# Kernel tuning notes

Hardware: AMD Instinct MI355X
Metric: run time of the kernel (lower is better)

## Reference

```python
import jax, jax.numpy as jnp
import numpy as np

# ---- problem constants (from init_kwargs) ----
R = 64
NX = 16384
NV = 2048
LX = 2.0
LV = 16.0
DX = LX / NX
DV = LV / NV
VS = (jnp.arange(NV, dtype=jnp.float32) + 0.5) * DV - LV / 2.0  # cell-centered v grid
AE, AI = 1.0, 100.0
ZE, ZI = -1.0, 1.0
OMEGA_C_TAU = 1.0
DT = 1e-3
SPECIES = ('electron', 'ion')
ZS = {'electron': ZE, 'ion': ZI}
AS = {'electron': AE, 'ion': AI}


def _minmod(a, b):
    return jnp.where(a * b > 0, jnp.where(jnp.abs(a) < jnp.abs(b), a, b), 0.0)


def slope_limited_flux_divergence(u, flux_func, dh):
    """u: (r, N+4) with 2 ghost cells each side; returns (r, N) flux divergence."""
    du = jnp.diff(u, axis=1)                    # (r, N+3)
    sigma = _minmod(du[:, :-1], du[:, 1:])      # slopes for cells 1..N+2, (r, N+2)
    uc = u[:, 1:-1]                             # cells 1..N+2
    left = uc[:, :-1] + 0.5 * sigma[:, :-1]     # interface states (r, N+1)
    right = uc[:, 1:] - 0.5 * sigma[:, 1:]
    F = flux_func(left, right)                  # (r, N+1)
    return (F[:, 1:] - F[:, :-1]) / dh


def apply_absorbing_wall_bcs(K, V, n_ghost):
    # V @ diag(indicator) @ V.T expressed as column-scaled GEMM
    Vm = (V * jnp.where(VS < 0, 1.0, 0.0)[None, :]) @ V.T * DV  # (r,r)
    Vp = (V * jnp.where(VS > 0, 1.0, 0.0)[None, :]) @ V.T * DV
    if n_ghost == 1:
        return jnp.concatenate([Vm @ K[:, :1], K, Vp @ K[:, -1:]], axis=1)
    return jnp.concatenate([Vm @ K[:, [1, 0]], K, Vp @ K[:, [-1, -2]]], axis=1)


def rho_c_species(X, S, V, Z):
    mass = V @ jnp.ones(NV, dtype=V.dtype) * DV   # (r,)
    return Z * (X.T @ (S @ mass))                  # (Nx,)


def poisson_solve(rho):
    # Periodic spectral Poisson: dE/dx = rho  ->  E_hat = rho_hat / (i k)
    k = 2.0 * jnp.pi * jnp.fft.fftfreq(NX, d=DX)
    rh = jnp.fft.fft(rho)
    Eh = jnp.where(k != 0, rh / (1j * k), 0.0)
    return jnp.real(jnp.fft.ifft(Eh)).astype(rho.dtype)


def solve_poisson(ys):
    rho = (rho_c_species(*ys['electron'], ZE) + rho_c_species(*ys['ion'], ZI))
    return poisson_solve(rho)


def ssprk2(y, f, dt):
    f0 = f(y)
    y1 = jax.tree.map(lambda a, b: a + dt * b, y, f0)
    f1 = f(y1)
    return jax.tree.map(lambda a, b, c: 0.5 * (a + b + dt * c), y, y1, f1)


def _vpm_matrices(V):
    vp = jnp.where(VS > 0, VS, 0.0)
    vm = jnp.where(VS < 0, VS, 0.0)
    v_plus = (V * vp[None, :]) @ V.T * DV
    v_minus = (V * vm[None, :]) @ V.T * DV
    return v_plus, v_minus


def _V_lr_matrices(V):
    dV = jnp.diff(V, axis=1) / DV
    zc = jnp.zeros((R, 1), dtype=V.dtype)
    V_left = V @ jnp.concatenate([zc, dV], axis=1).T * DV
    V_right = V @ jnp.concatenate([dV, zc], axis=1).T * DV
    return V_left, V_right


def K_rhs(K, V, E, Z, A):
    v_plus, v_minus = _vpm_matrices(V)
    V_left, V_right = _V_lr_matrices(V)
    Ep = jnp.where(E > 0, E, 0.0)[None, :]
    Em = jnp.where(E < 0, E, 0.0)[None, :]
    Kb = apply_absorbing_wall_bcs(K, V, 2)
    v_flux = slope_limited_flux_divergence(
        Kb, lambda l, r: v_plus @ l + v_minus @ r, DX)
    fac = OMEGA_C_TAU * Z / A
    E_flux = fac * (V_left @ (K * Ep) + V_right @ (K * Em))
    return -v_flux - E_flux


def _K_lr_matrices(X, S, V):
    K = apply_absorbing_wall_bcs((X.T @ S).T, V, 1)   # (r, Nx+2)
    Kdl = jnp.diff(K[:, :-1], axis=1) / DX            # (r, Nx)
    Kdr = jnp.diff(K[:, 1:], axis=1) / DX
    K_left = X @ Kdl.T * DX                           # (r, r)
    K_right = X @ Kdr.T * DX
    return K_left, K_right


def S_rhs(S, X, V, E, Z, A):
    v_plus, v_minus = _vpm_matrices(V)
    K_left, K_right = _K_lr_matrices(X, S, V)
    v_term = K_left @ v_plus.T + K_right @ v_minus.T
    V_left, V_right = _V_lr_matrices(V)
    Ep_mat = (X * jnp.where(E > 0, E, 0.0)[None, :]) @ X.T * DX
    Em_mat = (X * jnp.where(E < 0, E, 0.0)[None, :]) @ X.T * DX
    fac = OMEGA_C_TAU * Z / A
    E_term = fac * (Ep_mat @ S @ V_left.T + Em_mat @ S @ V_right.T)
    return v_term + E_term


def L_rhs(L, X, E, Z, A):
    Vt, S = jnp.linalg.qr(L.T)          # L.T: (Nv, r)
    S = S * DV ** 0.5
    V = Vt.T / DV ** 0.5
    K_left, K_right = _K_lr_matrices(X, S, V)
    vp = jnp.where(VS > 0, VS, 0.0)[None, :]
    vm = jnp.where(VS < 0, VS, 0.0)[None, :]
    v_flux = vp * (K_left @ V) + vm * (K_right @ V)
    fac = OMEGA_C_TAU * Z / A
    Ef = fac * E
    Ep_mat = (X * jnp.where(Ef > 0, Ef, 0.0)[None, :]) @ X.T * DX
    Em_mat = (X * jnp.where(Ef < 0, Ef, 0.0)[None, :]) @ X.T * DX
    Lb = jnp.pad(L, [(0, 0), (2, 2)])   # ghost cells (zeros in lieu of mode='empty')
    E_flux = slope_limited_flux_divergence(
        Lb, lambda l, r: Ep_mat @ l + Em_mat @ r, DV)
    return -v_flux - E_flux


def step(ys):
    # --- K step ---
    E = solve_poisson(ys)
    Ks = {sp: (ys[sp][0].T @ ys[sp][1]).T for sp in SPECIES}
    Ks = ssprk2(Ks, lambda Ks: {sp: K_rhs(Ks[sp], ys[sp][2], E, ZS[sp], AS[sp])
                                for sp in SPECIES}, DT)
    new = {}
    for sp in SPECIES:
        Xt, S = jnp.linalg.qr(Ks[sp].T)
        new[sp] = (Xt.T / DX ** 0.5, S * DX ** 0.5, ys[sp][2])
    ys = new
    # --- S step ---
    E = solve_poisson(ys)
    Ss = {sp: ys[sp][1] for sp in SPECIES}
    Ss = ssprk2(Ss, lambda Ss: {sp: S_rhs(Ss[sp], ys[sp][0], ys[sp][2], E, ZS[sp], AS[sp])
                                for sp in SPECIES}, DT)
    ys = {sp: (ys[sp][0], Ss[sp], ys[sp][2]) for sp in SPECIES}
    # --- L step ---
    E = solve_poisson(ys)
    Ls = {sp: ys[sp][1] @ ys[sp][2] for sp in SPECIES}
    Ls = ssprk2(Ls, lambda Ls: {sp: L_rhs(Ls[sp], ys[sp][0], E, ZS[sp], AS[sp])
                                for sp in SPECIES}, DT)
    new = {}
    for sp in SPECIES:
        Vt, S = jnp.linalg.qr(Ls[sp].T)
        new[sp] = (ys[sp][0], S * DV ** 0.5, Vt.T / DV ** 0.5)
    return new


def _ortho_rows(key, r, n, dh):
    A = jax.random.normal(key, (n, r), dtype=jnp.float32)
    Q, _ = jnp.linalg.qr(A)
    return Q.T / jnp.sqrt(dh)   # rows orthonormal w.r.t. trapezoid weight dh


def setup_inputs() -> dict:
    key = jax.random.key(0)
    ks = jax.random.split(key, 6)
    Xe = _ortho_rows(ks[0], R, NX, DX)
    Ve = _ortho_rows(ks[1], R, NV, DV)
    Xi = _ortho_rows(ks[2], R, NX, DX)
    Vi = _ortho_rows(ks[3], R, NV, DV)
    Se = 0.1 * jnp.eye(R, dtype=jnp.float32) + 0.01 * jax.random.normal(ks[4], (R, R), dtype=jnp.float32)
    Si = 0.1 * jnp.eye(R, dtype=jnp.float32) + 0.01 * jax.random.normal(ks[5], (R, R), dtype=jnp.float32)
    return {'Xe': Xe, 'Se': Se, 'Ve': Ve, 'Xi': Xi, 'Si': Si, 'Vi': Vi}


def reference(Xe, Se, Ve, Xi, Si, Vi):
    ys = {'electron': (Xe, Se, Ve), 'ion': (Xi, Si, Vi)}
    ys = step(ys)
    return (ys['electron'][0], ys['electron'][1], ys['electron'][2],
            ys['ion'][0], ys['ion'][1], ys['ion'][2])
```

## Files before the change

### kernel.cpp

```cpp
#include <hip/hip_runtime.h>

#define R 64
#define NX 16384
#define NV 2048
#define NXP (NX+8)
#define NVP (NV+8)
#define TW 64
#define SPLIT_VM 8
#define SPLIT_X 64
#define SPLIT_QRX 128
#define SPLIT_QRV 32

#define DXf 1.220703125e-4f
#define DVf 0.0078125f
#define DTf 0.001f
#define PI_F 3.14159265358979323846f
#define FAC_E (-1.0f)
#define FAC_I (0.01f)
#define ZE_F (-1.0f)
#define ZI_F (1.0f)
#define SQRT_DXf 0.011048543456039806f
#define SQRT_DVf 0.08838834764831845f
#define ISQRT_DXf 90.50966799187808f
#define ISQRT_DVf 11.313708498984761f

#define X_OFF 0
#define V_OFF 1048576
#define S_OFF 1179648
#define S1_OFF 1183744
#define SQ_OFF 1187840
#define D_OFF 1191936
#define MATS_OFF 1196032
#define SM_OFF 1228800
#define GLR_OFF 1245184
#define R1IF_OFF 1269760
#define KA_OFF 1277952
#define KB_OFF 2327040
#define LA_OFF KB_OFF
#define LB_OFF (KB_OFF+131584)
#define VQ_OFF (KB_OFF+394240)
#define PART_OFF 3376128
#define PARTQR_OFF PART_OFF
#define GD_OFF 4686848
#define SPS 4695040
#define RHO_OFF 9390080
#define E_OFF 9406464
#define C_OFF 9422848
#define FFT1_OFF 9426944
#define FFT2_OFF 9459712
#define DOUT_SPS 1183744
#define DOUT_X 0
#define DOUT_S 1048576
#define DOUT_V 1052672

__device__ __forceinline__ float mm2(float a, float b) {
    return (a*b > 0.0f) ? ((fabsf(a) < fabsf(b)) ? a : b) : 0.0f;
}

__global__ __launch_bounds__(256) void k_gram(float* W, int mode, int a_off, int lda,
    int e_abs, float fac0, float fac1, int out_off, int N, int nsplit)
{
  int sp = blockIdx.z, mat = blockIdx.y, split = blockIdx.x;
  float* base = W + (size_t)sp*SPS;
  const float* A = base + a_off;
  float fac = sp ? fac1 : fac0;
  float* outp = base + out_off + (size_t)(mat*nsplit + split)*4096;
  int chunk = N / nsplit;
  int xb0 = split * chunk;
  __shared__ float tA[TW][R+1], tB[TW][R+1];
  float acc[4][4] = {};
  int tid = threadIdx.x, ty = tid >> 4, tx = tid & 15;
  for (int xt = 0; xt < chunk; xt += TW) {
    for (int idx = tid; idx < TW*R; idx += 256) {
      int xi = idx & 63, r = idx >> 6;
      int x = xb0 + xt + xi;
      float av, bv;
      if (mode == 0) {
        float vv = A[(size_t)r*lda + x];
        float vs = ((float)x + 0.5f)*DVf - 8.0f;
        if (mat == 0)      { av = vv * (fmaxf(vs,0.f)*DVf); bv = vv; }
        else if (mat == 1) { av = vv * (fminf(vs,0.f)*DVf); bv = vv; }
        else if (mat == 2) { av = vv * ((vs<0.f)?DVf:0.f); bv = vv; }
        else if (mat == 3) { av = vv * ((vs>0.f)?DVf:0.f); bv = vv; }
        else if (mat == 4) { av = vv; bv = (x>=1)   ? (vv - A[(size_t)r*lda + x-1]) : 0.f; }
        else               { av = vv; bv = (x<NV-1) ? (A[(size_t)r*lda + x+1] - vv) : 0.f; }
      } else if (mode == 1) {
        float vv = A[(size_t)r*lda + x];
        float vs = ((float)x + 0.5f)*DVf - 8.0f;
        float w = (mat==0) ? ((vs<0.f)?DVf:0.f) : ((vs>0.f)?DVf:0.f);
        av = vv*w; bv = vv;
      } else if (mode == 3) {
        float e = W[e_abs + x] * fac;
        float vv = A[(size_t)r*lda + x];
        av = vv * (((mat==0) ? fmaxf(e,0.f) : fminf(e,0.f)) * DXf);
        bv = vv;
      } else {
        float vv = A[(size_t)r*lda + x];
        av = vv;
        if (mat == 0) bv = (x>=1)  ? (vv - A[(size_t)r*lda + x-1]) : vv;
        else          bv = (x<N-1) ? (A[(size_t)r*lda + x+1] - vv) : -vv;
      }
      tA[xi][r] = av; tB[xi][r] = bv;
    }
    __syncthreads();
    for (int xi = 0; xi < TW; ++xi) {
      float a0 = tA[xi][ty*4+0], a1 = tA[xi][ty*4+1], a2 = tA[xi][ty*4+2], a3 = tA[xi][ty*4+3];
      float b0 = tB[xi][tx*4+0], b1 = tB[xi][tx*4+1], b2 = tB[xi][tx*4+2], b3 = tB[xi][tx*4+3];
      acc[0][0]+=a0*b0; acc[0][1]+=a0*b1; acc[0][2]+=a0*b2; acc[0][3]+=a0*b3;
      acc[1][0]+=a1*b0; acc[1][1]+=a1*b1; acc[1][2]+=a1*b2; acc[1][3]+=a1*b3;
      acc[2][0]+=a2*b0; acc[2][1]+=a2*b1; acc[2][2]+=a2*b2; acc[2][3]+=a2*b3;
      acc[3][0]+=a3*b0; acc[3][1]+=a3*b1; acc[3][2]+=a3*b2; acc[3][3]+=a3*b3;
    }
    __syncthreads();
  }
  #pragma unroll
  for (int i = 0; i < 4; ++i)
    #pragma unroll
    for (int j = 0; j < 4; ++j)
      outp[(ty*4+i)*64 + tx*4 + j] = acc[i][j];
}

__global__ __launch_bounds__(256) void k_gram_qr(float* W, int a_off, int lda, int aoff,
    int N, int nsplit, int outd_off)
{
  int sp = blockIdx.z, split = blockIdx.x;
  float* base = W + (size_t)sp*SPS;
  const float* A = base + a_off + aoff;
  double* outp = (double*)(base + outd_off) + (size_t)split*4096;
  int chunk = N / nsplit, x0 = split*chunk;
  __shared__ float tA[TW][R+1];
  double acc[4][4] = {};
  int tid = threadIdx.x, ty = tid >> 4, tx = tid & 15;
  for (int xt = 0; xt < chunk; xt += TW) {
    for (int idx = tid; idx < TW*R; idx += 256) {
      int xi = idx & 63, r = idx >> 6;
      tA[xi][r] = A[(size_t)r*lda + x0 + xt + xi];
    }
    __syncthreads();
    for (int xi = 0; xi < TW; ++xi) {
      double a0 = tA[xi][ty*4+0], a1 = tA[xi][ty*4+1], a2 = tA[xi][ty*4+2], a3 = tA[xi][ty*4+3];
      double b0 = tA[xi][tx*4+0], b1 = tA[xi][tx*4+1], b2 = tA[xi][tx*4+2], b3 = tA[xi][tx*4+3];
      acc[0][0]+=a0*b0; acc[0][1]+=a0*b1; acc[0][2]+=a0*b2; acc[0][3]+=a0*b3;
      acc[1][0]+=a1*b0; acc[1][1]+=a1*b1; acc[1][2]+=a1*b2; acc[1][3]+=a1*b3;
      acc[2][0]+=a2*b0; acc[2][1]+=a2*b1; acc[2][2]+=a2*b2; acc[2][3]+=a2*b3;
      acc[3][0]+=a3*b0; acc[3][1]+=a3*b1; acc[3][2]+=a3*b2; acc[3][3]+=a3*b3;
    }
    __syncthreads();
  }
  #pragma unroll
  for (int i = 0; i < 4; ++i)
    #pragma unroll
    for (int j = 0; j < 4; ++j)
      outp[(ty*4+i)*64 + tx*4 + j] = acc[i][j];
}

__global__ __launch_bounds__(256) void k_reduce2(float* W, int src_off, int dst_off, int nsplit)
{
  int sp = blockIdx.z, mat = blockIdx.x;
  int e = blockIdx.y*256 + threadIdx.x;
  float* base = W + (size_t)sp*SPS;
  const float* src = base + src_off + (size_t)mat*nsplit*4096 + e;
  float s = 0;
  for (int k = 0; k < nsplit; ++k) s += src[(size_t)k*4096];
  base[dst_off + (size_t)mat*4096 + e] = s;
}

__global__ __launch_bounds__(256) void k_reduced(float* W, int src_off, int dst_off, int nsplit)
{
  int sp = blockIdx.z;
  int e = blockIdx.x*256 + threadIdx.x;
  float* base = W + (size_t)sp*SPS;
  const double* src = (const double*)(base + src_off) + e;
  double s = 0;
  for (int k = 0; k < nsplit; ++k) s += src[(size_t)k*4096];
  ((double*)(base + dst_off))[e] = s;
}

__global__ __launch_bounds__(256) void k_rr(float* W, int a_off, int transA, int b_off,
    int ldb, int boff, int c_off, int ldc, int coff, int d_off, float alpha,
    float* dout, int dmir_off)
{
  int sp = blockIdx.z;
  float* base = W + (size_t)sp*SPS;
  const float* A = base + a_off;
  const float* B = base + b_off + boff;
  float* C = base + c_off + coff;
  float* M = (dmir_off >= 0) ? (dout + (size_t)sp*DOUT_SPS + dmir_off) : nullptr;
  __shared__ float tA[R][R+1];
  __shared__ float dsc[R];
  int tid = threadIdx.x;
  for (int idx = tid; idx < R*R; idx += 256) {
    int r = idx >> 6, j = idx & 63;
    tA[r][j] = transA ? A[j*R + r] : A[idx];
  }
  if (tid < R) dsc[tid] = (d_off >= 0) ? base[d_off + tid] : 1.0f;
  __syncthreads();
  int ty = tid >> 4, tx = tid & 15;
  int x0 = blockIdx.x*64 + tx*4;
  float acc[4][4] = {};
  for (int r = 0; r < R; ++r) {
    float4 bv = *(const float4*)(B + (size_t)r*ldb + x0);
    float a0 = tA[r][ty*4+0], a1 = tA[r][ty*4+1], a2 = tA[r][ty*4+2], a3 = tA[r][ty*4+3];
    acc[0][0]+=a0*bv.x; acc[0][1]+=a0*bv.y; acc[0][2]+=a0*bv.z; acc[0][3]+=a0*bv.w;
    acc[1][0]+=a1*bv.x; acc[1][1]+=a1*bv.y; acc[1][2]+=a1*bv.z; acc[1][3]+=a1*bv.w;
    acc[2][0]+=a2*bv.x; acc[2][1]+=a2*bv.y; acc[2][2]+=a2*bv.z; acc[2][3]+=a2*bv.w;
    acc[3][0]+=a3*bv.x; acc[3][1]+=a3*bv.y; acc[3][2]+=a3*bv.z; acc[3][3]+=a3*bv.w;
  }
  #pragma unroll
  for (int i = 0; i < 4; ++i) {
    int j = ty*4 + i;
    float s = alpha * dsc[j];
    float4 o = make_float4(acc[i][0]*s, acc[i][1]*s, acc[i][2]*s, acc[i][3]*s);
    *(float4*)(C + (size_t)j*ldc + x0) = o;
    if (M) *(float4*)(M + (size_t)j*ldc + x0) = o;
  }
}

__global__ __launch_bounds__(256) void k_ghost2(float* W, int k_off)
{
  int sp = blockIdx.z;
  float* base = W + (size_t)sp*SPS;
  float* K = base + k_off;
  int tid = threadIdx.x;
  int j = tid & 63, c = tid >> 6;
  const float* M = base + MATS_OFF + ((c < 2) ? 2 : 3)*4096;
  int dst = (c==0)?2 : (c==1)?3 : (c==2)?(NX+4):(NX+5);
  int src = (c==0)?5 : (c==1)?4 : (c==2)?(NX+3):(NX+2);
  float s = 0;
  for (int m = 0; m < R; ++m) s += M[j*R + m] * K[(size_t)m*NXP + src];
  K[(size_t)j*NXP + dst] = s;
}

__global__ __launch_bounds__(256) void k_ghostL(float* W)
{
  int sp = blockIdx.z;
  float* base = W + (size_t)sp*SPS;
  for (int idx = threadIdx.x; idx < 512; idx += 256) {
    int which = idx >> 8; int r = (idx >> 2) & 63; int c = idx & 3;
    int col = (c < 2) ? (2 + c) : (NV + 4 + (c - 2));
    (base + (which ? LB_OFF : LA_OFF))[(size_t)r*NVP + col] = 0.f;
  }
}

__global__ __launch_bounds__(256) void k_flux(float* W, int U_off, int Kx_off, int ldkx,
    int kxoff, int useWin, int P_off, int Mi_off, int A2_off, int B2_off,
    int e_abs, float fac0, float fac1, float dh_inv, int N, int ldp,
    int stage, int orig_off, int out_off)
{
  int sp = blockIdx.z;
  float* base = W + (size_t)sp*SPS;
  const float* U  = base + U_off;
  const float* Kx = base + Kx_off;
  const float* Pm = base + P_off;
  const float* Mm = base + Mi_off;
  const float* Am = base + A2_off;
  const float* Bm = base + B2_off;
  float fac = sp ? fac1 : fac0;
  int x0 = blockIdx.x * 32;
  __shared__ float win[R][37];
  __shared__ float dLt[32][R+1];
  __shared__ float dRt[32][R+1];
  __shared__ float KTt[32][R+1];
  int tid = threadIdx.x;
  for (int idx = tid; idx < R*36; idx += 256) {
    int c = idx % 36, m = idx / 36;
    win[m][c] = U[(size_t)m*ldp + x0 + 2 + c];
  }
  __syncthreads();
  for (int idx = tid; idx < R*32; idx += 256) {
    int xi = idx & 31, m = idx >> 5;
    float u0 = win[m][xi], u1 = win[m][xi+1], u2 = win[m][xi+2], u3 = win[m][xi+3], u4 = win[m][xi+4];
    float d01 = u1-u0, d12 = u2-u1, d23 = u3-u2, d34 = u4-u3;
    float s1 = mm2(d01,d12), s2 = mm2(d12,d23), s3 = mm2(d23,d34);
    dLt[xi][m] = ((u2 + 0.5f*s2) - (u1 + 0.5f*s1)) * dh_inv;
    dRt[xi][m] = ((u3 - 0.5f*s3) - (u2 - 0.5f*s2)) * dh_inv;
    KTt[xi][m] = useWin ? u2 : Kx[(size_t)m*ldkx + kxoff + x0 + xi];
  }
  __syncthreads();
  int ty = tid >> 4, tx = tid & 15;
  int j0 = ty*4;
  float aP[4][2] = {}, aM[4][2] = {}, aA[4][2] = {}, aB[4][2] = {};
  for (int m = 0; m < R; ++m) {
    float dl0 = dLt[tx*2][m],   dl1 = dLt[tx*2+1][m];
    float dr0 = dRt[tx*2][m],   dr1 = dRt[tx*2+1][m];
    float kt0 = KTt[tx*2][m],   kt1 = KTt[tx*2+1][m];
    #pragma unroll
    for (int i = 0; i < 4; ++i) {
      float p = Pm[(j0+i)*R + m], q = Mm[(j0+i)*R + m];
      float a = Am[(j0+i)*R + m], b = Bm[(j0+i)*R + m];
      aP[i][0] += p*dl0; aP[i][1] += p*dl1;
      aM[i][0] += q*dr0; aM[i][1] += q*dr1;
      aA[i][0] += a*kt0; aA[i][1] += a*kt1;
      aB[i][0] += b*kt0; aB[i][1] += b*kt1;
    }
  }
  const float* orig = base + orig_off;
  float* out = base + out_off;
  for (int xx = 0; xx < 2; ++xx) {
    int x = x0 + tx*2 + xx;
    float w1, w2;
    if (e_abs >= 0) { float e = W[e_abs + x]; w1 = fac*fmaxf(e,0.f); w2 = fac*fminf(e,0.f); }
    else { float vs = ((float)x + 0.5f)*DVf - 8.0f; w1 = fmaxf(vs,0.f); w2 = fminf(vs,0.f); }
    #pragma unroll
    for (int i = 0; i < 4; ++i) {
      int j = j0 + i;
      float rhs = -(aP[i][xx] + aM[i][xx] + w1*aA[i][xx] + w2*aB[i][xx]);
      float uval = win[j][tx*2 + xx + 2];
      float res;
      if (stage == 1) res = uval + DTf*rhs;
      else res = 0.5f*(orig[(size_t)j*ldp + 4 + x] + uval + DTf*rhs);
      out[(size_t)j*ldp + 4 + x] = res;
    }
  }
}

__global__ __launch_bounds__(512) void k_cholA(float* W, int gd_off,
    int a_off, int lda, int aoff, int sout_off, float sscale,
    float* dout, int dmir_off)
{
  int sp = blockIdx.z;
  float* base = W + (size_t)sp*SPS;
  const double* GD = (const double*)(base + gd_off);
  const float* A = base + a_off + aoff;
  float* Rinv = base + R1IF_OFF;
  __shared__ double G[R][R+1];
  __shared__ double Wi[R][R+1];
  __shared__ double T[R][R+1];
  __shared__ float  As[R][R+1];
  __shared__ double Pb[32][33];
  __shared__ double red[8][R];
  __shared__ double dinv[R];
  __shared__ double dsh[R];
  int tid = threadIdx.x;
  int j = tid & 63, q = tid >> 6;
  for (int e = tid; e < 4096; e += 512) {
    G[e>>6][e&63] = GD[e];
    As[e>>6][e&63] = A[(size_t)(e>>6)*lda + (e&63)];
  }
  __syncthreads();
  for (int k = 0; k < R; ++k) {
    if (j > k) {
      double gkj = G[k][j] / G[k][k];
      for (int i = k+1+q; i <= j; i += 8) G[i][j] -= G[k][i]*gkj;
    }
    __syncthreads();
  }
  if (tid < R) dinv[tid] = 1.0 / sqrt(G[tid][tid]);
  __syncthreads();
  for (int i = q; i <= j; i += 8) G[i][j] *= dinv[i];
  __syncthreads();
  if (q == 0) Wi[j][j] = dinv[j];
  __syncthreads();
  int blo = j & 32;
  for (int t = 1; t < 32; ++t) {
    int i = j - t;
    double s = 0;
    if (i >= blo) {
      for (int m = i+1+q; m <= j; m += 8) s += G[i][m]*Wi[m][j];
    }
    red[q][j] = s;
    __syncthreads();
    if (q == 0 && i >= blo)
      Wi[i][j] = -(red[0][j]+red[1][j]+red[2][j]+red[3][j]
                  +red[4][j]+red[5][j]+red[6][j]+red[7][j]) * dinv[i];
    __syncthreads();
  }
  for (int u = 0; u < 2; ++u) {
    int e = tid + 512*u;
    int m = e >> 5, jj = 32 + (e & 31);
    double s = 0;
    for (int k2 = 32; k2 <= jj; ++k2) s += G[m][k2]*Wi[k2][jj];
    Pb[m][jj-32] = s;
  }
  __syncthreads();
  for (int u = 0; u < 2; ++u) {
    int e = tid + 512*u;
    int i = e >> 5, jj = 32 + (e & 31);
    double s = 0;
    for (int m = i; m < 32; ++m) s += Wi[i][m]*Pb[m][jj-32];
    Wi[i][jj] = -s;
  }
  __syncthreads();
  for (int e = tid; e < 4096; e += 512) {
    int i = e>>6, jj = e&63;
    Rinv[e] = (i<=jj) ? (float)Wi[i][jj] : 0.0f;
  }
  for (int x = q; x < R; x += 8) {
    double s = 0;
    for (int m = 0; m <= j; ++m) s += Wi[m][j]*(double)As[m][x];
    T[x][j] = s;
  }
  __syncthreads();
  for (int k = 0; k < R; ++k) {
    double tkk = T[k][k];
    double d = (tkk >= 0.0) ? -1.0 : 1.0;
    if (tid == k) dsh[k] = d;
    if (j > k) {
      double c = d * T[k][j] / (1.0 + fabs(tkk));
      for (int m = k+1+q; m < R; m += 8) T[m][j] += c * T[m][k];
    }
    __syncthreads();
  }
  if (tid < 64) base[D_OFF + tid] = (float)dsh[tid];
  float* mir = (dmir_off >= 0) ? (dout + (size_t)sp*DOUT_SPS + dmir_off) : nullptr;
  for (int e = tid; e < 4096; e += 512) {
    int i = e >> 6, jj = e & 63;
    float v = (i <= jj) ? (float)(dsh[i] * G[i][jj] * (double)sscale) : 0.0f;
    base[sout_off + e] = v;
    if (mir) mir[e] = v;
  }
}

__global__ __launch_bounds__(256) void k_klr(float* W, int s_off, int vm_idx, int vp_idx)
{
  int sp = blockIdx.x;
  float* base = W + (size_t)sp*SPS;
  __shared__ float Cb[4096];
  __shared__ float x0s[R], x1s[R], u0[R], u1[R], g0[R], g1[R];
  int tid = threadIdx.x, ty = tid>>4, tx = tid&15;
  const float* Sin = base + s_off;
  for (int e = tid; e < 4096; e += 256) Cb[e] = Sin[e];
  if (tid < R) { x0s[tid] = base[X_OFF + (size_t)tid*NX]; x1s[tid] = base[X_OFF + (size_t)tid*NX + NX-1]; }
  __syncthreads();
  if (tid < R) {
    float s0=0,s1=0;
    for (int m=0;m<R;++m){ float c=Cb[m*64+tid]; s0+=c*x0s[m]; s1+=c*x1s[m]; }
    u0[tid]=s0; u1[tid]=s1;
  }
  __syncthreads();
  if (tid < R) {
    const float* Vm = base + MATS_OFF + vm_idx*4096;
    const float* Vp = base + MATS_OFF + vp_idx*4096;
    float s0=0,s1=0;
    for (int c=0;c<R;++c){ s0+=Vm[tid*64+c]*u0[c]; s1+=Vp[tid*64+c]*u1[c]; }
    g0[tid]=s0; g1[tid]=s1;
  }
  __syncthreads();
  const float* GLg = base + GLR_OFF;
  const float* GRg = base + GLR_OFF + 4096;
  float aKL[4][4]={}, aKR[4][4]={};
  for (int m=0;m<R;++m) {
    float gl[4], gr[4], cj[4];
    #pragma unroll
    for (int i=0;i<4;++i){ gl[i]=GLg[(ty*4+i)*64+m]; gr[i]=GRg[(ty*4+i)*64+m]; }
    #pragma unroll
    for (int j=0;j<4;++j) cj[j]=Cb[m*64+tx*4+j];
    #pragma unroll
    for (int i=0;i<4;++i)
      #pragma unroll
      for (int j=0;j<4;++j){ aKL[i][j]+=gl[i]*cj[j]; aKR[i][j]+=gr[i]*cj[j]; }
  }
  #pragma unroll
  for (int i=0;i<4;++i)
    #pragma unroll
    for (int j=0;j<4;++j){
      int e=(ty*4+i)*64+tx*4+j;
      base[SM_OFF+e]      = aKL[i][j] - x0s[ty*4+i]*g0[tx*4+j];
      base[SM_OFF+4096+e] = aKR[i][j] + x1s[ty*4+i]*g1[tx*4+j];
    }
}

__global__ __launch_bounds__(256) void k_sstep(float* W, int stage)
{
  int sp = blockIdx.x;
  float* base = W + (size_t)sp*SPS;
  float fac = sp ? FAC_I : FAC_E;
  __shared__ float Ab[4096], Bb[4096], Cb[4096];
  __shared__ float x0s[R], x1s[R], u0[R], u1[R], g0[R], g1[R];
  int tid = threadIdx.x, ty = tid >> 4, tx = tid & 15;
  const float* Sin = base + ((stage==1)? S_OFF : S1_OFF);
  for (int e = tid; e < 4096; e += 256) Cb[e] = Sin[e];
  if (tid < R) { x0s[tid] = base[X_OFF + (size_t)tid*NX]; x1s[tid] = base[X_OFF + (size_t)tid*NX + NX-1]; }
  __syncthreads();
  if (tid < R) {
    float s0=0,s1=0;
    for (int m=0;m<R;++m){ float c=Cb[m*64+tid]; s0+=c*x0s[m]; s1+=c*x1s[m]; }
    u0[tid]=s0; u1[tid]=s1;
  }
  __syncthreads();
  if (tid < R) {
    const float* Vm = base + MATS_OFF + 2*4096;
    const float* Vp = base + MATS_OFF + 3*4096;
    float s0=0,s1=0;
    for (int c=0;c<R;++c){ s0+=Vm[tid*64+c]*u0[c]; s1+=Vp[tid*64+c]*u1[c]; }
    g0[tid]=s0; g1[tid]=s1;
  }
  __syncthreads();
  {
    const float* GLg = base + GLR_OFF;
    const float* GRg = base + GLR_OFF + 4096;
    float aKL[4][4]={}, aKR[4][4]={};
    for (int m=0;m<R;++m) {
      float gl[4], gr[4], cj[4];
      #pragma unroll
      for (int i=0;i<4;++i){ gl[i]=GLg[(ty*4+i)*64+m]; gr[i]=GRg[(ty*4+i)*64+m]; }
      #pragma unroll
      for (int j=0;j<4;++j) cj[j]=Cb[m*64+tx*4+j];
      #pragma unroll
      for (int i=0;i<4;++i)
        #pragma unroll
        for (int j=0;j<4;++j){ aKL[i][j]+=gl[i]*cj[j]; aKR[i][j]+=gr[i]*cj[j]; }
    }
    #pragma unroll
    for (int i=0;i<4;++i)
      #pragma unroll
      for (int j=0;j<4;++j){
        int e=(ty*4+i)*64+tx*4+j;
        Ab[e] = aKL[i][j] - x0s[ty*4+i]*g0[tx*4+j];
        Bb[e] = aKR[i][j] + x1s[ty*4+i]*g1[tx*4+j];
      }
  }
  __syncthreads();
  const float* vpm = base + MATS_OFF + 0*4096;
  const float* vmm = base + MATS_OFF + 1*4096;
  const float* vlm = base + MATS_OFF + 4*4096;
  const float* vrm = base + MATS_OFF + 5*4096;
  float accV[4][4] = {}, accE[4][4] = {};
  for (int m = 0; m < R; ++m) {
    float kl[4], kr[4], vpj[4], vmj[4];
    #pragma unroll
    for (int i = 0; i < 4; ++i) { kl[i] = Ab[(ty*4+i)*64+m]; kr[i] = Bb[(ty*4+i)*64+m]; }
    #pragma unroll
    for (int j = 0; j < 4; ++j) { vpj[j] = vpm[(tx*4+j)*64+m]; vmj[j] = vmm[(tx*4+j)*64+m]; }
    #pragma unroll
    for (int i = 0; i < 4; ++i)
      #pragma unroll
      for (int j = 0; j < 4; ++j)
        accV[i][j] += kl[i]*vpj[j] + kr[i]*vmj[j];
  }
  __syncthreads();
  for (int e = tid; e < 4096; e += 256) Ab[e] = base[SM_OFF + 2*4096 + e];
  __syncthreads();
  float t1[4][4] = {};
  for (int m = 0; m < R; ++m) {
    float ar[4], cj[4];
    #pragma unroll
    for (int i = 0; i < 4; ++i) ar[i] = Ab[(ty*4+i)*64+m];
    #pragma unroll
    for (int j = 0; j < 4; ++j) cj[j] = Cb[m*64 + tx*4+j];
    #pragma unroll
    for (int i = 0; i < 4; ++i)
      #pragma unroll
      for (int j = 0; j < 4; ++j) t1[i][j] += ar[i]*cj[j];
  }
  __syncthreads();
  #pragma unroll
  for (int i = 0; i < 4; ++i)
    #pragma unroll
    for (int j = 0; j < 4; ++j) Bb[(ty*4+i)*64 + tx*4+j] = t1[i][j];
  __syncthreads();
  for (int m = 0; m < R; ++m) {
    float ar[4], vj[4];
    #pragma unroll
    for (int i = 0; i < 4; ++i) ar[i] = Bb[(ty*4+i)*64+m];
    #pragma unroll
    for (int j = 0; j < 4; ++j) vj[j] = vlm[(tx*4+j)*64+m];
    #pragma unroll
    for (int i = 0; i < 4; ++i)
      #pragma unroll
      for (int j = 0; j < 4; ++j) accE[i][j] += ar[i]*vj[j];
  }
  __syncthreads();
  for (int e = tid; e < 4096; e += 256) Ab[e] = base[SM_OFF + 3*4096 + e];
  __syncthreads();
  float t2[4][4] = {};
  for (int m = 0; m < R; ++m) {
    float ar[4], cj[4];
    #pragma unroll
    for (int i = 0; i < 4; ++i) ar[i] = Ab[(ty*4+i)*64+m];
    #pragma unroll
    for (int j = 0; j < 4; ++j) cj[j] = Cb[m*64 + tx*4+j];
    #pragma unroll
    for (int i = 0; i < 4; ++i)
      #pragma unroll
      for (int j = 0; j < 4; ++j) t2[i][j] += ar[i]*cj[j];
  }
  __syncthreads();
  #pragma unroll
  for (int i = 0; i < 4; ++i)
    #pragma unroll
    for (int j = 0; j < 4; ++j) Bb[(ty*4+i)*64 + tx*4+j] = t2[i][j];
  __syncthreads();
  for (int m = 0; m < R; ++m) {
    float ar[4], vj[4];
    #pragma unroll
    for (int i = 0; i < 4; ++i) ar[i] = Bb[(ty*4+i)*64+m];
    #pragma unroll
    for (int j = 0; j < 4; ++j) vj[j] = vrm[(tx*4+j)*64+m];
    #pragma unroll
    for (int i = 0; i < 4; ++i)
      #pragma unroll
      for (int j = 0; j < 4; ++j) accE[i][j] += ar[i]*vj[j];
  }
  #pragma unroll
  for (int i = 0; i < 4; ++i)
    #pragma unroll
    for (int j = 0; j < 4; ++j) {
      int e = (ty*4+i)*64 + tx*4+j;
      float rhs = accV[i][j] + fac*accE[i][j];
      if (stage == 1) base[S1_OFF + e] = base[S_OFF + e] + DTf*rhs;
      else base[S_OFF + e] = 0.5f*(base[S_OFF + e] + base[S1_OFF + e] + DTf*rhs);
    }
}

__global__ __launch_bounds__(256) void k_csolve(float* W)
{
  int sp = blockIdx.x;
  float* base = W + (size_t)sp*SPS;
  const float* V = base + V_OFF;
  const float* S = base + S_OFF;
  __shared__ float red[R][4];
  __shared__ float mass[R];
  int tid = threadIdx.x;
  int r = tid >> 2, q = tid & 3;
  float s = 0;
  for (int v = q; v < NV; v += 4) s += V[(size_t)r*NV + v];
  red[r][q] = s;
  __syncthreads();
  if (tid < R) mass[tid] = (red[tid][0]+red[tid][1]+red[tid][2]+red[tid][3]) * DVf;
  __syncthreads();
  if (tid < R) {
    float c = 0;
    for (int j = 0; j < R; ++j) c += S[tid*R + j] * mass[j];
    W[C_OFF + sp*R + tid] = c * (sp ? ZI_F : ZE_F);
  }
}

__global__ __launch_bounds__(256) void k_rho(float* W)
{
  int x = blockIdx.x*256 + threadIdx.x;
  float s = 0;
  for (int r = 0; r < R; ++r) s += W[X_OFF + (size_t)r*NX + x] * W[C_OFF + r];
  for (int r = 0; r < R; ++r) s += W[(size_t)SPS + X_OFF + (size_t)r*NX + x] * W[C_OFF + R + r];
  W[RHO_OFF + x] = s;
}

__device__ inline void fft128fwd(float2* b, int t)
{
  __syncthreads();
  int r0 = (int)(__brev((unsigned)t) >> 25);
  int r1 = (int)(__brev((unsigned)(t+64)) >> 25);
  float2 a0 = b[r0], a1 = b[r1];
  __syncthreads();
  b[t] = a0; b[t+64] = a1;
  for (int s = 1; s <= 7; ++s) {
    __syncthreads();
    int half = 1 << (s-1);
    int jj = t & (half-1);
    int g  = t >> (s-1);
    int pos = (g << s) + jj;
    float ang = -2.0f*PI_F*(float)jj / (float)(1 << s);
    float sn, cs; sincosf(ang, &sn, &cs);
    float2 u = b[pos], wv = b[pos+half];
    float2 v = make_float2(wv.x*cs - wv.y*sn, wv.x*sn + wv.y*cs);
    b[pos] = make_float2(u.x+v.x, u.y+v.y);
    b[pos+half] = make_float2(u.x-v.x, u.y-v.y);
  }
}

__global__ __launch_bounds__(64) void k_fftA(float* W, int rin_off, int cin_off, int out_off)
{
  __shared__ float2 bb[128];
  int n1 = blockIdx.x, t = threadIdx.x;
  if (rin_off >= 0) {
    const float* rin = W + rin_off;
    bb[t]    = make_float2(rin[n1 + 128*t], 0.f);
    bb[t+64] = make_float2(rin[n1 + 128*(t+64)], 0.f);
  } else {
    const float2* cin = (const float2*)(W + cin_off);
    bb[t] = cin[n1 + 128*t]; bb[t+64] = cin[n1 + 128*(t+64)];
  }
  fft128fwd(bb, t);
  __syncthreads();
  float2* outp = (float2*)(W + out_off);
  for (int kk = 0; kk < 2; ++kk) {
    int k2 = t + 64*kk;
    float ang = -2.0f*PI_F*(float)(n1*k2) * (1.0f/16384.0f);
    float sn, cs; sincosf(ang, &sn, &cs);
    float2 v = bb[k2];
    outp[k2*128 + n1] = make_float2(v.x*cs - v.y*sn, v.x*sn + v.y*cs);
  }
}

__global__ __launch_bounds__(64) void k_fftB(float* W, int in_off, int out_off)
{
  __shared__ float2 bb[128];
  int k2 = blockIdx.x, t = threadIdx.x;
  const float2* in = (const float2*)(W + in_off);
  bb[t] = in[k2*128 + t]; bb[t+64] = in[k2*128 + t + 64];
  fft128fwd(bb, t);
  __syncthreads();
  float2* outp = (float2*)(W + out_off);
  for (int kk = 0; kk < 2; ++kk) {
    int k1 = t + 64*kk;
    int j = k2 + 128*k1;
    float2 X = bb[k1];
    float2 Hc;
    if (j == 0) Hc = make_float2(0.f, 0.f);
    else {
      float kphys = PI_F * (float)((j < 8192) ? j : (j - 16384));
      Hc = make_float2(X.y / kphys, X.x / kphys);
    }
    outp[j] = Hc;
  }
}

__global__ __launch_bounds__(64) void k_fftD(float* W, int in_off, int e_off)
{
  __shared__ float2 bb[128];
  int k2 = blockIdx.x, t = threadIdx.x;
  const float2* in = (const float2*)(W + in_off);
  bb[t] = in[k2*128 + t]; bb[t+64] = in[k2*128 + t + 64];
  fft128fwd(bb, t);
  __syncthreads();
  for (int kk = 0; kk < 2; ++kk) {
    int k1 = t + 64*kk;
    W[e_off + k2 + 128*k1] = bb[k1].x * (1.0f/16384.0f);
  }
}

extern "C" void kernel_launch(void* const* d_in, const int* in_sizes, int n_in,
                              void* d_out, int out_size, void* d_ws, size_t ws_size,
                              hipStream_t stream)
{
  float* W = (float*)d_ws;
  float* outp = (float*)d_out;
  const size_t FB = sizeof(float);
  hipMemcpyAsync(W + X_OFF, d_in[0], FB*(size_t)R*NX, hipMemcpyDeviceToDevice, stream);
  hipMemcpyAsync(W + S_OFF, d_in[1], FB*(size_t)R*R,  hipMemcpyDeviceToDevice, stream);
  hipMemcpyAsync(W + V_OFF, d_in[2], FB*(size_t)R*NV, hipMemcpyDeviceToDevice, stream);
  hipMemcpyAsync(W + (size_t)SPS + X_OFF, d_in[3], FB*(size_t)R*NX, hipMemcpyDeviceToDevice, stream);
  hipMemcpyAsync(W + (size_t)SPS + S_OFF, d_in[4], FB*(size_t)R*R,  hipMemcpyDeviceToDevice, stream);
  hipMemcpyAsync(W + (size_t)SPS + V_OFF, d_in[5], FB*(size_t)R*NV, hipMemcpyDeviceToDevice, stream);

  k_gram<<<dim3(SPLIT_VM,6,2),256,0,stream>>>(W, 0, V_OFF, NV, -1, 0.f,0.f, PART_OFF, NV, SPLIT_VM);
  k_reduce2<<<dim3(6,16,2),256,0,stream>>>(W, PART_OFF, MATS_OFF, SPLIT_VM);

  auto poisson = [&]() {
    k_csolve<<<dim3(2),256,0,stream>>>(W);
    k_rho<<<dim3(NX/256),256,0,stream>>>(W);
    k_fftA<<<dim3(128),64,0,stream>>>(W, RHO_OFF, -1, FFT1_OFF);
    k_fftB<<<dim3(128),64,0,stream>>>(W, FFT1_OFF, FFT2_OFF);
    k_fftA<<<dim3(128),64,0,stream>>>(W, -1, FFT2_OFF, FFT1_OFF);
    k_fftD<<<dim3(128),64,0,stream>>>(W, FFT1_OFF, E_OFF);
  };

  auto qr = [&](int a_off, int lda, int aoff, int N_, int nsplit,
                int sout_off, float sscale, int xout_off, int xout_ld, float inv_s,
                int smir, int xmir) {
    k_gram_qr<<<dim3(nsplit,1,2),256,0,stream>>>(W, a_off, lda, aoff, N_, nsplit, PARTQR_OFF);
    k_reduced<<<dim3(16,1,2),256,0,stream>>>(W, PARTQR_OFF, GD_OFF, nsplit);
    k_cholA<<<dim3(1,1,2),512,0,stream>>>(W, GD_OFF, a_off, lda, aoff, sout_off, sscale, outp, smir);
    k_rr<<<dim3(N_/64,1,2),256,0,stream>>>(W, R1IF_OFF, 0, a_off, lda, aoff, xout_off, xout_ld, 0, D_OFF, inv_s, outp, xmir);
  };

  poisson();
  k_rr<<<dim3(NX/64,1,2),256,0,stream>>>(W, S_OFF, 0, X_OFF, NX, 0, KA_OFF, NXP, 4, -1, 1.0f, nullptr, -1);
  k_ghost2<<<dim3(1,1,2),256,0,stream>>>(W, KA_OFF);
  k_flux<<<dim3(NX/32,1,2),256,0,stream>>>(W, KA_OFF, KA_OFF, NXP, 4, 1,
      MATS_OFF+0*4096, MATS_OFF+1*4096, MATS_OFF+4*4096, MATS_OFF+5*4096,
      E_OFF, FAC_E, FAC_I, 1.0f/DXf, NX, NXP, 1, 0, KB_OFF);
  k_ghost2<<<dim3(1,1,2),256,0,stream>>>(W, KB_OFF);
  k_flux<<<dim3(NX/32,1,2),256,0,stream>>>(W, KB_OFF, KB_OFF, NXP, 4, 1,
      MATS_OFF+0*4096, MATS_OFF+1*4096, MATS_OFF+4*4096, MATS_OFF+5*4096,
      E_OFF, FAC_E, FAC_I, 1.0f/DXf, NX, NXP, 2, KA_OFF, KA_OFF);
  qr(KA_OFF, NXP, 4, NX, SPLIT_QRX, S_OFF, SQRT_DXf, X_OFF, NX, ISQRT_DXf, -1, DOUT_X);

  k_gram<<<dim3(SPLIT_X,2,2),256,0,stream>>>(W, 5, X_OFF, NX, -1, 0.f,0.f, PART_OFF, NX, SPLIT_X);
  k_reduce2<<<dim3(2,16,2),256,0,stream>>>(W, PART_OFF, GLR_OFF, SPLIT_X);

  poisson();
  k_gram<<<dim3(SPLIT_X,2,2),256,0,stream>>>(W, 3, X_OFF, NX, E_OFF, 1.0f, 1.0f, PART_OFF, NX, SPLIT_X);
  k_reduce2<<<dim3(2,16,2),256,0,stream>>>(W, PART_OFF, SM_OFF + 2*4096, SPLIT_X);
  k_sstep<<<dim3(2),256,0,stream>>>(W, 1);
  k_sstep<<<dim3(2),256,0,stream>>>(W, 2);

  poisson();
  k_gram<<<dim3(SPLIT_X,2,2),256,0,stream>>>(W, 3, X_OFF, NX, E_OFF, FAC_E, FAC_I, PART_OFF, NX, SPLIT_X);
  k_reduce2<<<dim3(2,16,2),256,0,stream>>>(W, PART_OFF, SM_OFF + 2*4096, SPLIT_X);
  k_rr<<<dim3(NV/64,1,2),256,0,stream>>>(W, S_OFF, 1, V_OFF, NV, 0, LA_OFF, NVP, 4, -1, 1.0f, nullptr, -1);
  k_ghostL<<<dim3(1,1,2),256,0,stream>>>(W);
  auto leval = [&](int Lsrc, int stage, int Ldst, int Lorig) {
    qr(Lsrc, NVP, 4, NV, SPLIT_QRV, SQ_OFF, SQRT_DVf, VQ_OFF, NV, ISQRT_DVf, -1, -1);
    k_gram<<<dim3(SPLIT_VM,2,2),256,0,stream>>>(W, 1, VQ_OFF, NV, -1, 0.f,0.f, PART_OFF, NV, SPLIT_VM);
    k_reduce2<<<dim3(2,16,2),256,0,stream>>>(W, PART_OFF, MATS_OFF + 6*4096, SPLIT_VM);
    k_klr<<<dim3(2),256,0,stream>>>(W, SQ_OFF, 6, 7);
    k_flux<<<dim3(NV/32,1,2),256,0,stream>>>(W, Lsrc, VQ_OFF, NV, 0, 0,
        SM_OFF+2*4096, SM_OFF+3*4096, SM_OFF+0*4096, SM_OFF+1*4096,
        -1, 0.f, 0.f, 1.0f/DVf, NV, NVP, stage, Lorig, Ldst);
  };
  leval(LA_OFF, 1, LB_OFF, 0);
  leval(LB_OFF, 2, LA_OFF, LA_OFF);
  qr(LA_OFF, NVP, 4, NV, SPLIT_QRV, S_OFF, SQRT_DVf, V_OFF, NV, ISQRT_DVf, DOUT_S, DOUT_V);

  (void)in_sizes; (void)n_in; (void)out_size; (void)ws_size;
}
```

Baseline: 1.416 ms.

## Fold ghost-cell and copy kernels, restructure triangular inverse, cut small launches

Replaces the six device-to-device memcpys with one copy kernel and folds the ghost-cell fill kernels (K boundary via wall matrices, zero ghosts for L) into the edge blocks of the flux kernel. Mass is computed once and the coefficient solve is merged into the rho kernel, removing a launch per Poisson solve. The Cholesky kernel's triangular inverse is rewritten as small diagonal blocks followed by recursive doubling block merges, with fewer barriers, and a switch to skip sign fixing is added (always set on). The aim is fewer launches and shorter serial chains in a latency-bound pipeline, at the cost of extra edge-block work and a new reduction order in the inverse.

```diff
diff --git a/kernel.cpp b/kernel.cpp
--- a/kernel.cpp
+++ b/kernel.cpp
@@ -30,6 +30,7 @@
 #define S1_OFF 1183744
 #define SQ_OFF 1187840
 #define D_OFF 1191936
+#define MASS_OFF 1192000
 #define MATS_OFF 1196032
 #define SM_OFF 1228800
 #define GLR_OFF 1245184
@@ -45,16 +46,38 @@
 #define SPS 4695040
 #define RHO_OFF 9390080
 #define E_OFF 9406464
-#define C_OFF 9422848
 #define FFT1_OFF 9426944
 #define FFT2_OFF 9459712
 #define DOUT_SPS 1183744
 #define DOUT_X 0
 #define DOUT_S 1048576
 #define DOUT_V 1052672
+#define CP_NX4 262144
+#define CP_NR4 1024
+#define CP_NV4 32768
+#define CP_SP  295936
+#define CP_TOT 591872
 
 __device__ __forceinline__ float mm2(float a, float b) {
     return (a*b > 0.0f) ? ((fabsf(a) < fabsf(b)) ? a : b) : 0.0f;
+}
+
+__global__ __launch_bounds__(256) void k_copyin(float* W, const float* Xe, const float* Se,
+    const float* Ve, const float* Xi, const float* Si, const float* Vi)
+{
+  for (size_t idx = (size_t)blockIdx.x*256 + threadIdx.x; idx < CP_TOT; idx += (size_t)gridDim.x*256) {
+    int sp = idx >= CP_SP;
+    int e = (int)(idx - (size_t)sp*CP_SP);
+    const float* Xs = sp ? Xi : Xe;
+    const float* Ss = sp ? Si : Se;
+    const float* Vs = sp ? Vi : Ve;
+    float* base = W + (size_t)sp*SPS;
+    float4 v; float* dst;
+    if (e < CP_NX4)               { v = ((const float4*)Xs)[e];            dst = base + X_OFF + 4*(size_t)e; }
+    else if (e < CP_NX4+CP_NR4)   { int t = e-CP_NX4; v = ((const float4*)Ss)[t]; dst = base + S_OFF + 4*(size_t)t; }
+    else                          { int t = e-CP_NX4-CP_NR4; v = ((const float4*)Vs)[t]; dst = base + V_OFF + 4*(size_t)t; }
+    *(float4*)dst = v;
+  }
 }
 
 __global__ __launch_bounds__(256) void k_gram(float* W, int mode, int a_off, int lda,
@@ -216,36 +239,10 @@
   }
 }
 
-__global__ __launch_bounds__(256) void k_ghost2(float* W, int k_off)
-{
-  int sp = blockIdx.z;
-  float* base = W + (size_t)sp*SPS;
-  float* K = base + k_off;
-  int tid = threadIdx.x;
-  int j = tid & 63, c = tid >> 6;
-  const float* M = base + MATS_OFF + ((c < 2) ? 2 : 3)*4096;
-  int dst = (c==0)?2 : (c==1)?3 : (c==2)?(NX+4):(NX+5);
-  int src = (c==0)?5 : (c==1)?4 : (c==2)?(NX+3):(NX+2);
-  float s = 0;
-  for (int m = 0; m < R; ++m) s += M[j*R + m] * K[(size_t)m*NXP + src];
-  K[(size_t)j*NXP + dst] = s;
-}
-
-__global__ __launch_bounds__(256) void k_ghostL(float* W)
-{
-  int sp = blockIdx.z;
-  float* base = W + (size_t)sp*SPS;
-  for (int idx = threadIdx.x; idx < 512; idx += 256) {
-    int which = idx >> 8; int r = (idx >> 2) & 63; int c = idx & 3;
-    int col = (c < 2) ? (2 + c) : (NV + 4 + (c - 2));
-    (base + (which ? LB_OFF : LA_OFF))[(size_t)r*NVP + col] = 0.f;
-  }
-}
-
 __global__ __launch_bounds__(256) void k_flux(float* W, int U_off, int Kx_off, int ldkx,
     int kxoff, int useWin, int P_off, int Mi_off, int A2_off, int B2_off,
     int e_abs, float fac0, float fac1, float dh_inv, int N, int ldp,
-    int stage, int orig_off, int out_off)
+    int stage, int orig_off, int out_off, int gmode)
 {
   int sp = blockIdx.z;
   float* base = W + (size_t)sp*SPS;
@@ -267,6 +264,34 @@
     win[m][c] = U[(size_t)m*ldp + x0 + 2 + c];
   }
   __syncthreads();
+  bool left = (blockIdx.x == 0), right = (blockIdx.x == (unsigned)(N/32 - 1));
+  if (left || right) {
+    if (gmode == 1) {
+      if (tid < 128) {
+        int jj = tid & 63, c = tid >> 6;
+        if (left) {
+          const float* Mv = base + MATS_OFF + 2*4096;
+          int srcl = (c==0) ? 3 : 2;
+          float s = 0;
+          for (int m = 0; m < R; ++m) s += Mv[jj*R + m] * win[m][srcl];
+          win[jj][c] = s;
+        } else {
+          const float* Mv = base + MATS_OFF + 3*4096;
+          int srcl = (c==0) ? 33 : 32;
+          float s = 0;
+          for (int m = 0; m < R; ++m) s += Mv[jj*R + m] * win[m][srcl];
+          win[jj][34 + c] = s;
+        }
+      }
+    } else {
+      if (tid < 128) {
+        int jj = tid & 63, c = tid >> 6;
+        if (left) win[jj][c] = 0.f;
+        else      win[jj][34 + c] = 0.f;
+      }
+    }
+    __syncthreads();
+  }
   for (int idx = tid; idx < R*32; idx += 256) {
     int xi = idx & 31, m = idx >> 5;
     float u0 = win[m][xi], u1 = win[m][xi+1], u2 = win[m][xi+2], u3 = win[m][xi+3], u4 = win[m][xi+4];
@@ -316,7 +341,7 @@
 
 __global__ __launch_bounds__(512) void k_cholA(float* W, int gd_off,
     int a_off, int lda, int aoff, int sout_off, float sscale,
-    float* dout, int dmir_off)
+    float* dout, int dmir_off, int want_sign)
 {
   int sp = blockIdx.z;
   float* base = W + (size_t)sp*SPS;
@@ -328,14 +353,13 @@
   __shared__ double T[R][R+1];
   __shared__ float  As[R][R+1];
   __shared__ double Pb[32][33];
-  __shared__ double red[8][R];
   __shared__ double dinv[R];
   __shared__ double dsh[R];
   int tid = threadIdx.x;
   int j = tid & 63, q = tid >> 6;
   for (int e = tid; e < 4096; e += 512) {
     G[e>>6][e&63] = GD[e];
-    As[e>>6][e&63] = A[(size_t)(e>>6)*lda + (e&63)];
+    if (want_sign) As[e>>6][e&63] = A[(size_t)(e>>6)*lda + (e&63)];
   }
   __syncthreads();
   for (int k = 0; k < R; ++k) {
@@ -349,65 +373,74 @@
   __syncthreads();
   for (int i = q; i <= j; i += 8) G[i][j] *= dinv[i];
   __syncthreads();
-  if (q == 0) Wi[j][j] = dinv[j];
-  __syncthreads();
-  int blo = j & 32;
-  for (int t = 1; t < 32; ++t) {
-    int i = j - t;
-    double s = 0;
-    if (i >= blo) {
-      for (int m = i+1+q; m <= j; m += 8) s += G[i][m]*Wi[m][j];
-    }
-    red[q][j] = s;
-    __syncthreads();
-    if (q == 0 && i >= blo)
-      Wi[i][j] = -(red[0][j]+red[1][j]+red[2][j]+red[3][j]
-                  +red[4][j]+red[5][j]+red[6][j]+red[7][j]) * dinv[i];
-    __syncthreads();
-  }
-  for (int u = 0; u < 2; ++u) {
-    int e = tid + 512*u;
-    int m = e >> 5, jj = 32 + (e & 31);
-    double s = 0;
-    for (int k2 = 32; k2 <= jj; ++k2) s += G[m][k2]*Wi[k2][jj];
-    Pb[m][jj-32] = s;
-  }
-  __syncthreads();
-  for (int u = 0; u < 2; ++u) {
-    int e = tid + 512*u;
-    int i = e >> 5, jj = 32 + (e & 31);
-    double s = 0;
-    for (int m = i; m < 32; ++m) s += Wi[i][m]*Pb[m][jj-32];
-    Wi[i][jj] = -s;
-  }
-  __syncthreads();
+  if (tid < R) dinv[tid] = 1.0 / G[tid][tid];
+  __syncthreads();
+  if (q == 0) {
+    Wi[j][j] = dinv[j];
+    int blo = j & ~7;
+    for (int i = j-1; i >= blo; --i) {
+      double s = 0;
+      for (int m = i+1; m <= j; ++m) s += G[i][m]*Wi[m][j];
+      Wi[i][j] = -s * dinv[i];
+    }
+  }
+  __syncthreads();
+  for (int lg = 3; lg <= 5; ++lg) {
+    int n = 1 << lg;
+    int total = 32 << lg;
+    for (int e = tid; e < total; e += 512) {
+      int p = e >> (2*lg); int i = (e >> lg) & (n-1); int jj = e & (n-1);
+      int i0 = 2*n*p, j0 = i0 + n;
+      double s = 0;
+      for (int k2 = 0; k2 <= jj; ++k2) s += G[i0+i][j0+k2]*Wi[j0+k2][j0+jj];
+      Pb[p*n + i][jj] = s;
+    }
+    __syncthreads();
+    for (int e = tid; e < total; e += 512) {
+      int p = e >> (2*lg); int i = (e >> lg) & (n-1); int jj = e & (n-1);
+      int i0 = 2*n*p, j0 = i0 + n;
+      double s = 0;
+      for (int k2 = i; k2 < n; ++k2) s += Wi[i0+i][i0+k2]*Pb[p*n + k2][jj];
+      Wi[i0+i][j0+jj] = -s;
+    }
+    __syncthreads();
+  }
   for (int e = tid; e < 4096; e += 512) {
     int i = e>>6, jj = e&63;
     Rinv[e] = (i<=jj) ? (float)Wi[i][jj] : 0.0f;
   }
-  for (int x = q; x < R; x += 8) {
-    double s = 0;
-    for (int m = 0; m <= j; ++m) s += Wi[m][j]*(double)As[m][x];
-    T[x][j] = s;
-  }
-  __syncthreads();
-  for (int k = 0; k < R; ++k) {
-    double tkk = T[k][k];
-    double d = (tkk >= 0.0) ? -1.0 : 1.0;
-    if (tid == k) dsh[k] = d;
-    if (j > k) {
-      double c = d * T[k][j] / (1.0 + fabs(tkk));
-      for (int m = k+1+q; m < R; m += 8) T[m][j] += c * T[m][k];
-    }
-    __syncthreads();
-  }
-  if (tid < 64) base[D_OFF + tid] = (float)dsh[tid];
   float* mir = (dmir_off >= 0) ? (dout + (size_t)sp*DOUT_SPS + dmir_off) : nullptr;
-  for (int e = tid; e < 4096; e += 512) {
-    int i = e >> 6, jj = e & 63;
-    float v = (i <= jj) ? (float)(dsh[i] * G[i][jj] * (double)sscale) : 0.0f;
-    base[sout_off + e] = v;
-    if (mir) mir[e] = v;
+  if (want_sign) {
+    for (int x = q; x < R; x += 8) {
+      double s = 0;
+      for (int m = 0; m <= j; ++m) s += Wi[m][j]*(double)As[m][x];
+      T[x][j] = s;
+    }
+    __syncthreads();
+    for (int k = 0; k < R; ++k) {
+      double tkk = T[k][k];
+      double d = (tkk >= 0.0) ? -1.0 : 1.0;
+      if (tid == k) dsh[k] = d;
+      if (j > k) {
+        double c = d * T[k][j] / (1.0 + fabs(tkk));
+        for (int m = k+1+q; m < R; m += 8) T[m][j] += c * T[m][k];
+      }
+      __syncthreads();
+    }
+    if (tid < 64) base[D_OFF + tid] = (float)dsh[tid];
+    for (int e = tid; e < 4096; e += 512) {
+      int i = e >> 6, jj = e & 63;
+      float v = (i <= jj) ? (float)(dsh[i] * G[i][jj] * (double)sscale) : 0.0f;
+      base[sout_off + e] = v;
+      if (mir) mir[e] = v;
+    }
+  } else {
+    for (int e = tid; e < 4096; e += 512) {
+      int i = e >> 6, jj = e & 63;
+      float v = (i <= jj) ? (float)(G[i][jj] * (double)sscale) : 0.0f;
+      base[sout_off + e] = v;
+      if (mir) mir[e] = v;
+    }
   }
 }
 
@@ -603,35 +636,38 @@
     }
 }
 
-__global__ __launch_bounds__(256) void k_csolve(float* W)
+__global__ __launch_bounds__(256) void k_mass(float* W)
 {
   int sp = blockIdx.x;
   float* base = W + (size_t)sp*SPS;
   const float* V = base + V_OFF;
-  const float* S = base + S_OFF;
   __shared__ float red[R][4];
-  __shared__ float mass[R];
   int tid = threadIdx.x;
   int r = tid >> 2, q = tid & 3;
   float s = 0;
   for (int v = q; v < NV; v += 4) s += V[(size_t)r*NV + v];
   red[r][q] = s;
   __syncthreads();
-  if (tid < R) mass[tid] = (red[tid][0]+red[tid][1]+red[tid][2]+red[tid][3]) * DVf;
-  __syncthreads();
-  if (tid < R) {
+  if (tid < R) base[MASS_OFF + tid] = (red[tid][0]+red[tid][1]+red[tid][2]+red[tid][3]) * DVf;
+}
+
+__global__ __launch_bounds__(256) void k_rho(float* W)
+{
+  __shared__ float cs[2][R];
+  int tid = threadIdx.x;
+  if (tid < 128) {
+    int sp = tid >> 6, r = tid & 63;
+    const float* S = W + (size_t)sp*SPS + S_OFF;
+    const float* ms = W + (size_t)sp*SPS + MASS_OFF;
     float c = 0;
-    for (int j = 0; j < R; ++j) c += S[tid*R + j] * mass[j];
-    W[C_OFF + sp*R + tid] = c * (sp ? ZI_F : ZE_F);
-  }
-}
-
-__global__ __launch_bounds__(256) void k_rho(float* W)
-{
-  int x = blockIdx.x*256 + threadIdx.x;
+    for (int jj = 0; jj < R; ++jj) c += S[r*R + jj] * ms[jj];
+    cs[sp][r] = c * (sp ? ZI_F : ZE_F);
+  }
+  __syncthreads();
+  int x = blockIdx.x*256 + tid;
   float s = 0;
-  for (int r = 0; r < R; ++r) s += W[X_OFF + (size_t)r*NX + x] * W[C_OFF + r];
-  for (int r = 0; r < R; ++r) s += W[(size_t)SPS + X_OFF + (size_t)r*NX + x] * W[C_OFF + R + r];
+  for (int r = 0; r < R; ++r) s += W[X_OFF + (size_t)r*NX + x] * cs[0][r];
+  for (int r = 0; r < R; ++r) s += W[(size_t)SPS + X_OFF + (size_t)r*NX + x] * cs[1][r];
   W[RHO_OFF + x] = s;
 }
 
@@ -725,19 +761,14 @@
 {
   float* W = (float*)d_ws;
   float* outp = (float*)d_out;
-  const size_t FB = sizeof(float);
-  hipMemcpyAsync(W + X_OFF, d_in[0], FB*(size_t)R*NX, hipMemcpyDeviceToDevice, stream);
-  hipMemcpyAsync(W + S_OFF, d_in[1], FB*(size_t)R*R,  hipMemcpyDeviceToDevice, stream);
-  hipMemcpyAsync(W + V_OFF, d_in[2], FB*(size_t)R*NV, hipMemcpyDeviceToDevice, stream);
-  hipMemcpyAsync(W + (size_t)SPS + X_OFF, d_in[3], FB*(size_t)R*NX, hipMemcpyDeviceToDevice, stream);
-  hipMemcpyAsync(W + (size_t)SPS + S_OFF, d_in[4], FB*(size_t)R*R,  hipMemcpyDeviceToDevice, stream);
-  hipMemcpyAsync(W + (size_t)SPS + V_OFF, d_in[5], FB*(size_t)R*NV, hipMemcpyDeviceToDevice, stream);
+  k_copyin<<<1024,256,0,stream>>>(W, (const float*)d_in[0], (const float*)d_in[1],
+      (const float*)d_in[2], (const float*)d_in[3], (const float*)d_in[4], (const float*)d_in[5]);
 
   k_gram<<<dim3(SPLIT_VM,6,2),256,0,stream>>>(W, 0, V_OFF, NV, -1, 0.f,0.f, PART_OFF, NV, SPLIT_VM);
   k_reduce2<<<dim3(6,16,2),256,0,stream>>>(W, PART_OFF, MATS_OFF, SPLIT_VM);
+  k_mass<<<dim3(2),256,0,stream>>>(W);
 
   auto poisson = [&]() {
-    k_csolve<<<dim3(2),256,0,stream>>>(W);
     k_rho<<<dim3(NX/256),256,0,stream>>>(W);
     k_fftA<<<dim3(128),64,0,stream>>>(W, RHO_OFF, -1, FFT1_OFF);
     k_fftB<<<dim3(128),64,0,stream>>>(W, FFT1_OFF, FFT2_OFF);
@@ -750,20 +781,19 @@
                 int smir, int xmir) {
     k_gram_qr<<<dim3(nsplit,1,2),256,0,stream>>>(W, a_off, lda, aoff, N_, nsplit, PARTQR_OFF);
     k_reduced<<<dim3(16,1,2),256,0,stream>>>(W, PARTQR_OFF, GD_OFF, nsplit);
-    k_cholA<<<dim3(1,1,2),512,0,stream>>>(W, GD_OFF, a_off, lda, aoff, sout_off, sscale, outp, smir);
-    k_rr<<<dim3(N_/64,1,2),256,0,stream>>>(W, R1IF_OFF, 0, a_off, lda, aoff, xout_off, xout_ld, 0, D_OFF, inv_s, outp, xmir);
+    k_cholA<<<dim3(1,1,2),512,0,stream>>>(W, GD_OFF, a_off, lda, aoff, sout_off, sscale, outp, smir, 1);
+    k_rr<<<dim3(N_/64,1,2),256,0,stream>>>(W, R1IF_OFF, 0, a_off, lda, aoff, xout_off, xout_ld, 0,
+                                           D_OFF, inv_s, outp, xmir);
   };
 
   poisson();
   k_rr<<<dim3(NX/64,1,2),256,0,stream>>>(W, S_OFF, 0, X_OFF, NX, 0, KA_OFF, NXP, 4, -1, 1.0f, nullptr, -1);
-  k_ghost2<<<dim3(1,1,2),256,0,stream>>>(W, KA_OFF);
   k_flux<<<dim3(NX/32,1,2),256,0,stream>>>(W, KA_OFF, KA_OFF, NXP, 4, 1,
       MATS_OFF+0*4096, MATS_OFF+1*4096, MATS_OFF+4*4096, MATS_OFF+5*4096,
-      E_OFF, FAC_E, FAC_I, 1.0f/DXf, NX, NXP, 1, 0, KB_OFF);
-  k_ghost2<<<dim3(1,1,2),256,0,stream>>>(W, KB_OFF);
+      E_OFF, FAC_E, FAC_I, 1.0f/DXf, NX, NXP, 1, 0, KB_OFF, 1);
   k_flux<<<dim3(NX/32,1,2),256,0,stream>>>(W, KB_OFF, KB_OFF, NXP, 4, 1,
       MATS_OFF+0*4096, MATS_OFF+1*4096, MATS_OFF+4*4096, MATS_OFF+5*4096,
-      E_OFF, FAC_E, FAC_I, 1.0f/DXf, NX, NXP, 2, KA_OFF, KA_OFF);
+      E_OFF, FAC_E, FAC_I, 1.0f/DXf, NX, NXP, 2, KA_OFF, KA_OFF, 1);
   qr(KA_OFF, NXP, 4, NX, SPLIT_QRX, S_OFF, SQRT_DXf, X_OFF, NX, ISQRT_DXf, -1, DOUT_X);
 
   k_gram<<<dim3(SPLIT_X,2,2),256,0,stream>>>(W, 5, X_OFF, NX, -1, 0.f,0.f, PART_OFF, NX, SPLIT_X);
@@ -779,7 +809,6 @@
   k_gram<<<dim3(SPLIT_X,2,2),256,0,stream>>>(W, 3, X_OFF, NX, E_OFF, FAC_E, FAC_I, PART_OFF, NX, SPLIT_X);
   k_reduce2<<<dim3(2,16,2),256,0,stream>>>(W, PART_OFF, SM_OFF + 2*4096, SPLIT_X);
   k_rr<<<dim3(NV/64,1,2),256,0,stream>>>(W, S_OFF, 1, V_OFF, NV, 0, LA_OFF, NVP, 4, -1, 1.0f, nullptr, -1);
-  k_ghostL<<<dim3(1,1,2),256,0,stream>>>(W);
   auto leval = [&](int Lsrc, int stage, int Ldst, int Lorig) {
     qr(Lsrc, NVP, 4, NV, SPLIT_QRV, SQ_OFF, SQRT_DVf, VQ_OFF, NV, ISQRT_DVf, -1, -1);
     k_gram<<<dim3(SPLIT_VM,2,2),256,0,stream>>>(W, 1, VQ_OFF, NV, -1, 0.f,0.f, PART_OFF, NV, SPLIT_VM);
@@ -787,7 +816,7 @@
     k_klr<<<dim3(2),256,0,stream>>>(W, SQ_OFF, 6, 7);
     k_flux<<<dim3(NV/32,1,2),256,0,stream>>>(W, Lsrc, VQ_OFF, NV, 0, 0,
         SM_OFF+2*4096, SM_OFF+3*4096, SM_OFF+0*4096, SM_OFF+1*4096,
-        -1, 0.f, 0.f, 1.0f/DVf, NV, NVP, stage, Lorig, Ldst);
+        -1, 0.f, 0.f, 1.0f/DVf, NV, NVP, stage, Lorig, Ldst, 0);
   };
   leval(LA_OFF, 1, LB_OFF, 0);
   leval(LB_OFF, 2, LA_OFF, LA_OFF);
```

Result: faster. 1.288 ms (-9.0%).
